# Optimization experiments

Hardware: AMD Instinct MI355X
Metric: run time of the kernel (lower is better)

## Reference

```python
import jax, jax.numpy as jnp
import numpy as np

# pywt db4 reconstruction filters (wavelet.rec_lo / wavelet.rec_hi)
REC_LO = np.array([0.23037781330885523, 0.7148465705525415, 0.6308807679295904,
                   -0.02798376941698385, -0.18703481171888114, 0.030841381835986965,
                   0.032883011666982945, -0.010597401784997278], dtype=np.float32)
REC_HI = np.array([-0.010597401784997278, -0.032883011666982945, 0.030841381835986965,
                   0.18703481171888114, -0.02798376941698385, -0.6308807679295904,
                   0.7148465705525415, -0.23037781330885523], dtype=np.float32)

# coefficient lengths for signal N=262144, db4 (f=8), 6 levels, mode='zero'
_LENS = {'a': 4102, 'd6': 4102, 'd5': 8198, 'd4': 16390, 'd3': 32774, 'd2': 65541, 'd1': 131075}
_B = 128


def _idwt_step(a, d, rec_lo, rec_hi):
    """One pywt idwt level (zero mode): upsample-by-2 + filter-bank synthesis.
    a, d: (B, n) -> (B, 2n - f + 2).
    Upsample (zeros between samples, len 2n-1), full convolution with the
    reconstruction filters, trim f-2 samples each side == lhs_dilation=2 with
    padding (1, 1) in a cross-correlation with flipped kernels."""
    lhs = jnp.stack([a, d], axis=1)                              # (B, 2, n)
    rhs = jnp.stack([rec_lo[::-1], rec_hi[::-1]], axis=0)[None]  # (1, 2, f) OIH
    out = jax.lax.conv_general_dilated(
        lhs, rhs, window_strides=(1,), padding=[(1, 1)],
        lhs_dilation=(2,), dimension_numbers=('NCH', 'OIH', 'NCH'))
    return out[:, 0, :]


def _waverec(a, details, rec_lo, rec_hi):
    x = a
    for d in details:  # coarsest -> finest, matching pywt.waverec
        if x.shape[-1] == d.shape[-1] + 1:  # pywt crop-by-one rule (static)
            x = x[:, :-1]
        x = _idwt_step(x, d, rec_lo, rec_hi)
    return x


def setup_inputs() -> dict:
    key = jax.random.key(0)
    keys = jax.random.split(key, len(_LENS))
    return {name: jax.random.normal(k, (_B, n), dtype=jnp.float32)
            for k, (name, n) in zip(keys, _LENS.items())}


def reference(a, d6, d5, d4, d3, d2, d1):
    rec_lo = jnp.asarray(REC_LO)
    rec_hi = jnp.asarray(REC_HI)
    return _waverec(a, (d6, d5, d4, d3, d2, d1), rec_lo, rec_hi)  # (B, 262144)
```

## Files before the change

### kernel.cpp

```cpp
#include <hip/hip_runtime.h>

#define LO0 0.23037781330885523f
#define LO1 0.7148465705525415f
#define LO2 0.6308807679295904f
#define LO3 -0.02798376941698385f
#define LO4 -0.18703481171888114f
#define LO5 0.030841381835986965f
#define LO6 0.032883011666982945f
#define LO7 -0.010597401784997278f

#define HI0 -0.010597401784997278f
#define HI1 -0.032883011666982945f
#define HI2 0.030841381835986965f
#define HI3 0.18703481171888114f
#define HI4 -0.02798376941698385f
#define HI5 -0.6308807679295904f
#define HI6 0.7148465705525415f
#define HI7 -0.23037781330885523f

#define NT 256


__device__ __forceinline__ void synth_pair(
    float x0, float x1, float x2, float x3,
    float g0, float g1, float g2, float g3,
    float& e, float& o)
{
    e = x0 * LO6 + g0 * HI6;
    e = fmaf(x1, LO4, e); e = fmaf(g1, HI4, e);
    e = fmaf(x2, LO2, e); e = fmaf(g2, HI2, e);
    e = fmaf(x3, LO0, e); e = fmaf(g3, HI0, e);
    o = x0 * LO7 + g0 * HI7;
    o = fmaf(x1, LO5, o); o = fmaf(g1, HI5, o);
    o = fmaf(x2, LO3, o); o = fmaf(g2, HI3, o);
    o = fmaf(x3, LO1, o); o = fmaf(g3, HI1, o);
}

__device__ __forceinline__ void synth_group4_lds(
    const float* __restrict__ XB, const float* __restrict__ D,
    float* __restrict__ OB, int p0)
{
    float4 x0 = *reinterpret_cast<const float4*>(XB + p0);
    float4 x1 = *reinterpret_cast<const float4*>(XB + p0 + 4);
    float4 g0 = *reinterpret_cast<const float4*>(D + p0);
    float4 g1 = *reinterpret_cast<const float4*>(D + p0 + 4);
    float e0,o0,e1,o1,e2,o2,e3,o3;
    synth_pair(x0.x,x0.y,x0.z,x0.w, g0.x,g0.y,g0.z,g0.w, e0,o0);
    synth_pair(x0.y,x0.z,x0.w,x1.x, g0.y,g0.z,g0.w,g1.x, e1,o1);
    synth_pair(x0.z,x0.w,x1.x,x1.y, g0.z,g0.w,g1.x,g1.y, e2,o2);
    synth_pair(x0.w,x1.x,x1.y,x1.z, g0.w,g1.x,g1.y,g1.z, e3,o3);
    *reinterpret_cast<float4*>(OB + 2*p0)     = make_float4(e0,o0,e1,o1);
    *reinterpret_cast<float4*>(OB + 2*p0 + 4) = make_float4(e2,o2,e3,o3);
}

__device__ __forceinline__ void synth_group4_reg(
    const float* __restrict__ XB, int p0, const float* g, float* __restrict__ OB)
{
    float4 x0 = *reinterpret_cast<const float4*>(XB + p0);
    float4 x1 = *reinterpret_cast<const float4*>(XB + p0 + 4);
    float e0,o0,e1,o1,e2,o2,e3,o3;
    synth_pair(x0.x,x0.y,x0.z,x0.w, g[0],g[1],g[2],g[3], e0,o0);
    synth_pair(x0.y,x0.z,x0.w,x1.x, g[1],g[2],g[3],g[4], e1,o1);
    synth_pair(x0.z,x0.w,x1.x,x1.y, g[2],g[3],g[4],g[5], e2,o2);
    synth_pair(x0.w,x1.x,x1.y,x1.z, g[3],g[4],g[5],g[6], e3,o3);
    *reinterpret_cast<float4*>(OB + 2*p0)     = make_float4(e0,o0,e1,o1);
    *reinterpret_cast<float4*>(OB + 2*p0 + 4) = make_float4(e2,o2,e3,o3);
}

template<int NP>
__device__ __forceinline__ void wave_level(
    const float* __restrict__ XB, const float* __restrict__ D,
    float* __restrict__ OB, int lane)
{
    constexpr int NVEC = NP & ~3;
    static_assert(NVEC <= 256, "one vec group per lane");
    if (4 * lane < NVEC) synth_group4_lds(XB, D, OB, 4 * lane);
    if constexpr (NVEC < NP) {
        int p = NVEC + lane;
        if (p < NP) {
            float e, o;
            synth_pair(XB[p],XB[p+1],XB[p+2],XB[p+3],
                       D[p],D[p+1],D[p+2],D[p+3], e, o);
            OB[2*p]   = e;
            OB[2*p+1] = o;
        }
    }
}

typedef const __attribute__((address_space(1))) unsigned int* as1_u32_cptr;
typedef __attribute__((address_space(3))) unsigned int* as3_u32_ptr;

__device__ __forceinline__ void stage_async_w(const float* __restrict__ g,
                                              float* __restrict__ l,
                                              int n, int lane)
{
    for (int i = lane; i < n; i += 64) {
        __builtin_amdgcn_global_load_lds((as1_u32_cptr)(g + i),
                                         (as3_u32_ptr)(l + i), 4, 0, 0);
    }
}

__global__ __launch_bounds__(NT) void idwt_fused_kernel(
    const float* __restrict__ a,
    const float* __restrict__ d6, const float* __restrict__ d5,
    const float* __restrict__ d4, const float* __restrict__ d3,
    const float* __restrict__ d2, const float* __restrict__ d1,
    float* __restrict__ out)
{
    __shared__ __align__(16) float sA[4][264];
    __shared__ __align__(16) float sB[4][520];
    __shared__ __align__(16) float sD6[4][24];
    __shared__ __align__(16) float sD5[4][40];
    __shared__ __align__(16) float sD4[4][72];
    __shared__ __align__(16) float sD3[4][136];

    const int row  = blockIdx.y;
    const int wid  = threadIdx.x >> 6;
    const int lane = threadIdx.x & 63;
    const int K0w  = blockIdx.x * 4096 + wid * 1024;

    const float* pa  = a  + (long long)row * 4102   + (K0w >> 6);
    const float* pd6 = d6 + (long long)row * 4102   + (K0w >> 6);
    const float* pd5 = d5 + (long long)row * 8198   + (K0w >> 5);
    const float* pd4 = d4 + (long long)row * 16390  + (K0w >> 4);
    const float* pd3 = d3 + (long long)row * 32774  + (K0w >> 3);
    const float* pd2 = d2 + (long long)row * 65541  + (K0w >> 2);
    const float* pd1 = d1 + (long long)row * 131075 + (K0w >> 1);

    stage_async_w(pa,  sA[wid],  22,  lane);
    stage_async_w(pd6, sD6[wid], 22,  lane);
    stage_async_w(pd5, sD5[wid], 38,  lane);
    stage_async_w(pd4, sD4[wid], 70,  lane);
    stage_async_w(pd3, sD3[wid], 134, lane);

    float d2r[7];
#pragma unroll
    for (int j = 0; j < 7; ++j) d2r[j] = pd2[4 * lane + j];
    float d2t[4];
    if (lane < 2) {
#pragma unroll
        for (int j = 0; j < 4; ++j) d2t[j] = pd2[256 + lane + j];
    }

    asm volatile("s_waitcnt vmcnt(0)" ::: "memory");

    if (lane < 19) {
        float e, o;
        synth_pair(sA[wid][lane], sA[wid][lane+1], sA[wid][lane+2], sA[wid][lane+3],
                   sD6[wid][lane], sD6[wid][lane+1], sD6[wid][lane+2], sD6[wid][lane+3],
                   e, o);
        sB[wid][2*lane]   = e;
        sB[wid][2*lane+1] = o;
    }

    float d1A[7], d1B[7];
#pragma unroll
    for (int j = 0; j < 7; ++j) d1A[j] = pd1[4 * lane + j];
#pragma unroll
    for (int j = 0; j < 7; ++j) d1B[j] = pd1[4 * lane + 256 + j];

    wave_level<35> (sB[wid], sD5[wid], sA[wid], lane);
    wave_level<67> (sA[wid], sD4[wid], sB[wid], lane);
    wave_level<131>(sB[wid], sD3[wid], sA[wid], lane);

    synth_group4_reg(sA[wid], 4 * lane, d2r, sB[wid]);
    if (lane < 2) {
        int p = 256 + lane;
        float e, o;
        synth_pair(sA[wid][p], sA[wid][p+1], sA[wid][p+2], sA[wid][p+3],
                   d2t[0], d2t[1], d2t[2], d2t[3], e, o);
        sB[wid][2*p]   = e;
        sB[wid][2*p+1] = o;
    }

    float* orow = out + (long long)row * 262144 + K0w;
    synth_group4_reg(sB[wid], 4 * lane,       d1A, orow);
    synth_group4_reg(sB[wid], 4 * lane + 256, d1B, orow);
}

extern "C" void kernel_launch(void* const* d_in, const int* in_sizes, int n_in,
                              void* d_out, int out_size, void* d_ws, size_t ws_size,
                              hipStream_t stream) {
    const float* a  = (const float*)d_in[0];
    const float* d6 = (const float*)d_in[1];
    const float* d5 = (const float*)d_in[2];
    const float* d4 = (const float*)d_in[3];
    const float* d3 = (const float*)d_in[4];
    const float* d2 = (const float*)d_in[5];
    const float* d1 = (const float*)d_in[6];

    float* OUT = (float*)d_out;

    dim3 block(NT);
    dim3 grid(64, 128);
    idwt_fused_kernel<<<grid, block, 0, stream>>>(a, d6, d5, d4, d3, d2, d1, OUT);
}
```

Measured before the change: 48.76 us.

## Process four tiles per wave with register double-buffered prefetch of next tile

Each wave now handles four consecutive 1024-sample output tiles of the same row instead of one. While it computes the current tile, it prefetches the next tile's coarse coefficients into registers and its d2/d1 values into a second register set. The async global-to-LDS loads are replaced by plain register loads followed by LDS stores. The grid shrinks fourfold and the launch bounds now request 4 blocks per SIMD. The aim is to hide global load latency behind compute, at the cost of more registers and lower parallelism.

After: 64.63 us. +32.6%, slower.

```diff
diff --git a/kernel.cpp b/kernel.cpp
--- a/kernel.cpp
+++ b/kernel.cpp
@@ -87,20 +87,77 @@
     }
 }
 
-typedef const __attribute__((address_space(1))) unsigned int* as1_u32_cptr;
-typedef __attribute__((address_space(3))) unsigned int* as3_u32_ptr;
-
-__device__ __forceinline__ void stage_async_w(const float* __restrict__ g,
-                                              float* __restrict__ l,
-                                              int n, int lane)
-{
-    for (int i = lane; i < n; i += 64) {
-        __builtin_amdgcn_global_load_lds((as1_u32_cptr)(g + i),
-                                         (as3_u32_ptr)(l + i), 4, 0, 0);
-    }
-}
-
-__global__ __launch_bounds__(NT) void idwt_fused_kernel(
+struct StageRegs { float a0, g6, g5, g4a, g4b, g3a, g3b, g3c; };
+
+__device__ __forceinline__ void stage_load(
+    const float* pa, const float* pd6, const float* pd5, const float* pd4,
+    const float* pd3, StageRegs& S, int lane)
+{
+    if (lane < 22) { S.a0 = pa[lane]; S.g6 = pd6[lane]; }
+    if (lane < 38) S.g5 = pd5[lane];
+    S.g4a = pd4[lane];
+    if (lane < 6) S.g4b = pd4[64 + lane];
+    S.g3a = pd3[lane];
+    S.g3b = pd3[64 + lane];
+    if (lane < 6) S.g3c = pd3[128 + lane];
+}
+
+__device__ __forceinline__ void stage_write(
+    float* A, float* D6, float* D5, float* D4, float* D3,
+    const StageRegs& S, int lane)
+{
+    if (lane < 22) { A[lane] = S.a0; D6[lane] = S.g6; }
+    if (lane < 38) D5[lane] = S.g5;
+    D4[lane] = S.g4a;
+    if (lane < 6) D4[64 + lane] = S.g4b;
+    D3[lane] = S.g3a;
+    D3[64 + lane] = S.g3b;
+    if (lane < 6) D3[128 + lane] = S.g3c;
+}
+
+struct Regs { float d2r[7], d2t[4], d1A[7], d1B[7]; };
+
+__device__ __forceinline__ void load_regs(
+    const float* pd2, const float* pd1, Regs& R, int lane)
+{
+#pragma unroll
+    for (int j = 0; j < 7; ++j) R.d2r[j] = pd2[4 * lane + j];
+    if (lane < 2) {
+#pragma unroll
+        for (int j = 0; j < 4; ++j) R.d2t[j] = pd2[256 + lane + j];
+    }
+#pragma unroll
+    for (int j = 0; j < 7; ++j) R.d1A[j] = pd1[4 * lane + j];
+#pragma unroll
+    for (int j = 0; j < 7; ++j) R.d1B[j] = pd1[4 * lane + 256 + j];
+}
+
+__device__ __forceinline__ void compute_tile(
+    float* A, float* B, const float* D6, const float* D5, const float* D4,
+    const float* D3, const Regs& R, float* orow, int lane)
+{
+    if (lane < 19) {
+        float e, o;
+        synth_pair(A[lane],A[lane+1],A[lane+2],A[lane+3],
+                   D6[lane],D6[lane+1],D6[lane+2],D6[lane+3], e, o);
+        B[2*lane] = e; B[2*lane+1] = o;
+    }
+    wave_level<35> (B, D5, A, lane);
+    wave_level<67> (A, D4, B, lane);
+    wave_level<131>(B, D3, A, lane);
+    synth_group4_reg(A, 4 * lane, R.d2r, B);
+    if (lane < 2) {
+        int p = 256 + lane;
+        float e, o;
+        synth_pair(A[p],A[p+1],A[p+2],A[p+3],
+                   R.d2t[0],R.d2t[1],R.d2t[2],R.d2t[3], e, o);
+        B[2*p] = e; B[2*p+1] = o;
+    }
+    synth_group4_reg(B, 4 * lane,       R.d1A, orow);
+    synth_group4_reg(B, 4 * lane + 256, R.d1B, orow);
+}
+
+__global__ __launch_bounds__(NT, 4) void idwt_fused_kernel(
     const float* __restrict__ a,
     const float* __restrict__ d6, const float* __restrict__ d5,
     const float* __restrict__ d4, const float* __restrict__ d3,
@@ -114,68 +171,48 @@
     __shared__ __align__(16) float sD4[4][72];
     __shared__ __align__(16) float sD3[4][136];
 
-    const int row  = blockIdx.y;
     const int wid  = threadIdx.x >> 6;
     const int lane = threadIdx.x & 63;
-    const int K0w  = blockIdx.x * 4096 + wid * 1024;
-
-    const float* pa  = a  + (long long)row * 4102   + (K0w >> 6);
-    const float* pd6 = d6 + (long long)row * 4102   + (K0w >> 6);
-    const float* pd5 = d5 + (long long)row * 8198   + (K0w >> 5);
-    const float* pd4 = d4 + (long long)row * 16390  + (K0w >> 4);
-    const float* pd3 = d3 + (long long)row * 32774  + (K0w >> 3);
-    const float* pd2 = d2 + (long long)row * 65541  + (K0w >> 2);
-    const float* pd1 = d1 + (long long)row * 131075 + (K0w >> 1);
-
-    stage_async_w(pa,  sA[wid],  22,  lane);
-    stage_async_w(pd6, sD6[wid], 22,  lane);
-    stage_async_w(pd5, sD5[wid], 38,  lane);
-    stage_async_w(pd4, sD4[wid], 70,  lane);
-    stage_async_w(pd3, sD3[wid], 134, lane);
-
-    float d2r[7];
-#pragma unroll
-    for (int j = 0; j < 7; ++j) d2r[j] = pd2[4 * lane + j];
-    float d2t[4];
-    if (lane < 2) {
-#pragma unroll
-        for (int j = 0; j < 4; ++j) d2t[j] = pd2[256 + lane + j];
-    }
-
-    asm volatile("s_waitcnt vmcnt(0)" ::: "memory");
-
-    if (lane < 19) {
-        float e, o;
-        synth_pair(sA[wid][lane], sA[wid][lane+1], sA[wid][lane+2], sA[wid][lane+3],
-                   sD6[wid][lane], sD6[wid][lane+1], sD6[wid][lane+2], sD6[wid][lane+3],
-                   e, o);
-        sB[wid][2*lane]   = e;
-        sB[wid][2*lane+1] = o;
-    }
-
-    float d1A[7], d1B[7];
-#pragma unroll
-    for (int j = 0; j < 7; ++j) d1A[j] = pd1[4 * lane + j];
-#pragma unroll
-    for (int j = 0; j < 7; ++j) d1B[j] = pd1[4 * lane + 256 + j];
-
-    wave_level<35> (sB[wid], sD5[wid], sA[wid], lane);
-    wave_level<67> (sA[wid], sD4[wid], sB[wid], lane);
-    wave_level<131>(sB[wid], sD3[wid], sA[wid], lane);
-
-    synth_group4_reg(sA[wid], 4 * lane, d2r, sB[wid]);
-    if (lane < 2) {
-        int p = 256 + lane;
-        float e, o;
-        synth_pair(sA[wid][p], sA[wid][p+1], sA[wid][p+2], sA[wid][p+3],
-                   d2t[0], d2t[1], d2t[2], d2t[3], e, o);
-        sB[wid][2*p]   = e;
-        sB[wid][2*p+1] = o;
-    }
-
-    float* orow = out + (long long)row * 262144 + K0w;
-    synth_group4_reg(sB[wid], 4 * lane,       d1A, orow);
-    synth_group4_reg(sB[wid], 4 * lane + 256, d1B, orow);
+    const int wg   = blockIdx.x * 4 + wid;
+    const int row  = wg >> 6;
+    const int col0 = (wg & 63) << 12;
+
+    const float* ra  = a  + (long long)row * 4102   + (col0 >> 6);
+    const float* rd6 = d6 + (long long)row * 4102   + (col0 >> 6);
+    const float* rd5 = d5 + (long long)row * 8198   + (col0 >> 5);
+    const float* rd4 = d4 + (long long)row * 16390  + (col0 >> 4);
+    const float* rd3 = d3 + (long long)row * 32774  + (col0 >> 3);
+    const float* rd2 = d2 + (long long)row * 65541  + (col0 >> 2);
+    const float* rd1 = d1 + (long long)row * 131075 + (col0 >> 1);
+    float* orow = out + (long long)row * 262144 + col0;
+
+    StageRegs S;
+    Regs R0, R1;
+
+    stage_load(ra, rd6, rd5, rd4, rd3, S, lane);
+    load_regs(rd2, rd1, R0, lane);
+    stage_write(sA[wid], sD6[wid], sD5[wid], sD4[wid], sD3[wid], S, lane);
+
+#define STEP(t, CUR, NXT, IS_LAST)                                            \
+    {                                                                         \
+        if (!(IS_LAST)) {                                                     \
+            constexpr int u = (t) + 1;                                        \
+            stage_load(ra + 16*u, rd6 + 16*u, rd5 + 32*u, rd4 + 64*u,         \
+                       rd3 + 128*u, S, lane);                                 \
+            load_regs(rd2 + 256*u, rd1 + 512*u, NXT, lane);                   \
+        }                                                                     \
+        compute_tile(sA[wid], sB[wid], sD6[wid], sD5[wid], sD4[wid],          \
+                     sD3[wid], CUR, orow + 1024 * (t), lane);                 \
+        if (!(IS_LAST))                                                       \
+            stage_write(sA[wid], sD6[wid], sD5[wid], sD4[wid], sD3[wid],      \
+                        S, lane);                                             \
+    }
+
+    STEP(0, R0, R1, false)
+    STEP(1, R1, R0, false)
+    STEP(2, R0, R1, false)
+    STEP(3, R1, R0, true)
+#undef STEP
 }
 
 extern "C" void kernel_launch(void* const* d_in, const int* in_sizes, int n_in,
@@ -192,6 +229,6 @@
     float* OUT = (float*)d_out;
 
     dim3 block(NT);
-    dim3 grid(64, 128);
+    dim3 grid(2048);
     idwt_fused_kernel<<<grid, block, 0, stream>>>(a, d6, d5, d4, d3, d2, d1, OUT);
 }
```
